# Performance work log

Measured on AMD Instinct MI355X. Metric: run time of the kernel, lower is better.

Reference implementation:

```python
import jax, jax.numpy as jnp
import numpy as np

T, N, HIDDEN = 2048, 4, 512
N_HEAD = 8
D_HEAD = HIDDEN // N_HEAD
# Faithful to torch buffer: 1.0 / hidden_size ** d_head -> underflows to 0.0
SCALE = np.float32(1.0 / (HIDDEN ** D_HEAD))
LN_EPS = 1e-5


def _layernorm(x, g, b):
    m = jnp.mean(x, axis=-1, keepdims=True)
    v = jnp.mean(jnp.square(x - m), axis=-1, keepdims=True)
    return (x - m) * jax.lax.rsqrt(v + LN_EPS) * g + b


def setup_inputs() -> dict:
    key = jax.random.key(0)
    ks = jax.random.split(key, 6)
    s = 0.02
    return {
        "x": jax.random.normal(ks[0], (T, N, HIDDEN), jnp.float32),
        "qkv_w": jax.random.normal(ks[1], (HIDDEN, 3 * HIDDEN), jnp.float32) * s,
        "qkv_b": jnp.zeros((3 * HIDDEN,), jnp.float32),
        "out_w": jax.random.normal(ks[2], (HIDDEN, HIDDEN), jnp.float32) * s,
        "out_b": jnp.zeros((HIDDEN,), jnp.float32),
        "ln1_g": jnp.ones((HIDDEN,), jnp.float32),
        "ln1_b": jnp.zeros((HIDDEN,), jnp.float32),
        "ff1_w": jax.random.normal(ks[3], (HIDDEN, 2 * HIDDEN), jnp.float32) * s,
        "ff1_b": jnp.zeros((2 * HIDDEN,), jnp.float32),
        "ff2_w": jax.random.normal(ks[4], (2 * HIDDEN, HIDDEN), jnp.float32) * s,
        "ff2_b": jnp.zeros((HIDDEN,), jnp.float32),
        "ln2_g": jnp.ones((HIDDEN,), jnp.float32),
        "ln2_b": jnp.zeros((HIDDEN,), jnp.float32),
    }


def reference(x, qkv_w, qkv_b, out_w, out_b, ln1_g, ln1_b,
              ff1_w, ff1_b, ff2_w, ff2_b, ln2_g, ln2_b):
    t, n, _ = x.shape
    # prenorm=True path, dropout_p=0 (identity)
    residual = x
    h = _layernorm(x, ln1_g, ln1_b)
    qkv = h @ qkv_w + qkv_b  # [t, n, 3*hidden]
    q, k, v = jnp.split(qkv, 3, axis=2)
    q = q.reshape(t, n, N_HEAD, D_HEAD)
    k = k.reshape(t, n, N_HEAD, D_HEAD)
    v = v.reshape(t, n, N_HEAD, D_HEAD)
    logits = jnp.einsum('ibhd,jbhd->ijbh', q, k)
    probs = jax.nn.softmax(logits * SCALE, axis=1)
    attn_out = jnp.einsum('ijbh,jbhd->ibhd', probs, v).reshape(t, n, HIDDEN)
    x = residual + (attn_out @ out_w + out_b)
    residual = x
    h = _layernorm(x, ln2_g, ln2_b)
    ff = jnp.maximum(h @ ff1_w + ff1_b, 0.0) @ ff2_w + ff2_b
    return residual + ff
```

## Files before the change

### kernel.cpp

```cpp
#include <hip/hip_runtime.h>
#include <math.h>


#define DEVI __device__ __forceinline__

typedef unsigned short u16;
typedef unsigned int   u32;
using short8 = __attribute__((ext_vector_type(8))) short;
using f32x4  = __attribute__((ext_vector_type(4))) float;

constexpr int T_ = 2048;
constexpr int NB = 4;
constexpr int H  = 512;
constexpr int M  = T_ * NB;
constexpr int FF = 2 * H;
constexpr float LN_EPS = 1e-5f;
constexpr int NCHUNK = 256;

DEVI u16 f2bf(float f) {
    union { float f; u32 u; } v; v.f = f;
    u32 r = v.u + 0x7FFFu + ((v.u >> 16) & 1u);
    return (u16)(r >> 16);
}
DEVI float bf2f(u16 h) {
    union { u32 u; float f; } v; v.u = ((u32)h) << 16; return v.f;
}

DEVI void gload16(const u16* src, u16* lds) {
    __builtin_amdgcn_global_load_lds(
        (const __attribute__((address_space(1))) u32*)src,
        (__attribute__((address_space(3))) u32*)lds, 16, 0, 0);
}

DEVI float hsum8(const float4& a, const float4& b) {
    return a.x + a.y + a.z + a.w + b.x + b.y + b.z + b.w;
}
DEVI float hsq8(const float4& a, const float4& b) {
    return a.x*a.x + a.y*a.y + a.z*a.z + a.w*a.w +
           b.x*b.x + b.y*b.y + b.z*b.z + b.w*b.w;
}
DEVI float4 ln_apply(const float4& v, float mean, float rs,
                     const float4& g, const float4& b) {
    float4 r;
    r.x = (v.x - mean) * rs * g.x + b.x;
    r.y = (v.y - mean) * rs * g.y + b.y;
    r.z = (v.z - mean) * rs * g.z + b.z;
    r.w = (v.w - mean) * rs * g.w + b.w;
    return r;
}
DEVI void add4(float4& a, const float4& b) {
    a.x += b.x; a.y += b.y; a.z += b.z; a.w += b.w;
}
DEVI void wave_reduce2(float& s, float& q) {
    #pragma unroll
    for (int m = 1; m < 64; m <<= 1) {
        s += __shfl_xor(s, m, 64);
        q += __shfl_xor(q, m, 64);
    }
}

__global__ __launch_bounds__(256) void k_ln1_partial(
    const float* __restrict__ x, const float* __restrict__ g,
    const float* __restrict__ be, float* __restrict__ partials)
{
    const int lane = threadIdx.x & 63;
    const int w    = threadIdx.x >> 6;
    const int t0   = blockIdx.x * 8;

    const float4* G4 = (const float4*)g;
    const float4* B4 = (const float4*)be;
    const float4 g0 = G4[lane], g1 = G4[64 + lane];
    const float4 b0 = B4[lane], b1 = B4[64 + lane];

    float4 acc0 = {0, 0, 0, 0}, acc1 = {0, 0, 0, 0};
    for (int i = 0; i < 8; ++i) {
        const int r = (t0 + i) * NB + w;
        const float4* X4 = (const float4*)(x + (size_t)r * H);
        float4 v0 = X4[lane], v1 = X4[64 + lane];
        float s = hsum8(v0, v1);
        float q = hsq8(v0, v1);
        wave_reduce2(s, q);
        const float mean = s * (1.0f / H);
        const float var  = q * (1.0f / H) - mean * mean;
        const float rs   = 1.0f / sqrtf(var + LN_EPS);
        add4(acc0, ln_apply(v0, mean, rs, g0, b0));
        add4(acc1, ln_apply(v1, mean, rs, g1, b1));
    }
    float4* P4 = (float4*)(partials + ((size_t)w * NCHUNK + blockIdx.x) * H);
    P4[lane]      = acc0;
    P4[64 + lane] = acc1;
}

__global__ void k_reduce_mean(const float* __restrict__ partials,
                              float* __restrict__ mean_h1)
{
    const int tid = blockIdx.x * blockDim.x + threadIdx.x;
    const int b = tid >> 9;
    const int e = tid & 511;
    float s = 0.f;
    for (int c = 0; c < NCHUNK; ++c)
        s += partials[((size_t)b * NCHUNK + c) * H + e];
    mean_h1[tid] = s * (1.0f / T_);
}

__global__ __launch_bounds__(256) void k_gemv_wave(
    const float* __restrict__ vec, const float* __restrict__ W,
    const float* __restrict__ bias, float* __restrict__ outv,
    const int Kd, const int rowstride, const int colofs)
{
    const int wid  = blockIdx.x * 4 + (threadIdx.x >> 6);
    const int lane = threadIdx.x & 63;
    const int b = wid >> 9;
    const int j = wid & 511;
    const float* v  = vec + (size_t)b * Kd;
    const float* wc = W + colofs + j;
    float s = 0.f;
    for (int i = 0; i < Kd / 64; ++i) {
        const int k = i * 64 + lane;
        s = fmaf(v[k], wc[(size_t)k * rowstride], s);
    }
    #pragma unroll
    for (int m = 1; m < 64; m <<= 1) s += __shfl_xor(s, m, 64);
    if (lane == 0) outv[wid] = s + bias[j];
}

__global__ __launch_bounds__(256) void k_ln2(
    const float* __restrict__ x, const float* __restrict__ cvec,
    const float* __restrict__ g, const float* __restrict__ be,
    u16* __restrict__ h2bf)
{
    const int lane = threadIdx.x & 63;
    const int w    = threadIdx.x >> 6;
    const int r    = blockIdx.x * 4 + w;
    const int b    = r & 3;

    const float4* X4 = (const float4*)(x + (size_t)r * H);
    const float4* C4 = (const float4*)(cvec + (size_t)b * H);
    float4 v0 = X4[lane], v1 = X4[64 + lane];
    add4(v0, C4[lane]);
    add4(v1, C4[64 + lane]);

    float s = hsum8(v0, v1);
    float q = hsq8(v0, v1);
    wave_reduce2(s, q);
    const float mean = s * (1.0f / H);
    const float var  = q * (1.0f / H) - mean * mean;
    const float rs   = 1.0f / sqrtf(var + LN_EPS);

    const float4* G4 = (const float4*)g;
    const float4* B4 = (const float4*)be;
    float4 h0 = ln_apply(v0, mean, rs, G4[lane],      B4[lane]);
    float4 h1 = ln_apply(v1, mean, rs, G4[64 + lane], B4[64 + lane]);

    u16* row = h2bf + (size_t)r * H;
    *(ushort4*)&row[lane * 4]       = make_ushort4(f2bf(h0.x), f2bf(h0.y), f2bf(h0.z), f2bf(h0.w));
    *(ushort4*)&row[256 + lane * 4] = make_ushort4(f2bf(h1.x), f2bf(h1.y), f2bf(h1.z), f2bf(h1.w));
}

__global__ __launch_bounds__(256) void k_wsplit(
    const float* __restrict__ W, u16* __restrict__ Whi, u16* __restrict__ Wlo,
    const int K, const int N)
{
    __shared__ float tile[32][33];
    const int kt = blockIdx.x * 32, nt = blockIdx.y * 32;
    const int t = threadIdx.x;
    #pragma unroll
    for (int i = 0; i < 4; ++i) {
        const int idx = t + i * 256;
        const int r = idx >> 5, c = idx & 31;
        tile[r][c] = W[(size_t)(kt + r) * N + nt + c];
    }
    __syncthreads();
    #pragma unroll
    for (int i = 0; i < 4; ++i) {
        const int idx = t + i * 256;
        const int r = idx >> 5, c = idx & 31;
        const float v = tile[c][r];
        const u16 hi = f2bf(v);
        const u16 lo = f2bf(v - bf2f(hi));
        const size_t o = (size_t)(nt + r) * K + kt + c;
        Whi[o] = hi;
        Wlo[o] = lo;
    }
}

template<int BM, int BN, int MODE>
__global__ __launch_bounds__(256) void gemm_bf16(
    const u16* __restrict__ Abf, const u16* __restrict__ Bhi,
    const u16* __restrict__ Blo, const float* __restrict__ bias,
    const float* __restrict__ resid_x, const float* __restrict__ resid_c,
    float* __restrict__ outf, u16* __restrict__ outbf,
    const int K, const int N)
{
    constexpr int BK = 32;
    constexpr int WM = BM / 2, WN = BN / 2;
    constexpr int FM = WM / 16, FN = WN / 16;
    __shared__ alignas(16) u16 As[BM * BK];
    __shared__ alignas(16) u16 Bh[BN * BK];
    __shared__ alignas(16) u16 Bl[BN * BK];

    const int t    = threadIdx.x;
    const int lane = t & 63, w = t >> 6;
    const int wr = w >> 1, wc = w & 1;
    const int lr = lane & 15, lk = lane >> 4;
    const int bm0 = blockIdx.x * BM, bn0 = blockIdx.y * BN;

    f32x4 acc[FM][FN];
    #pragma unroll
    for (int i = 0; i < FM; ++i)
        #pragma unroll
        for (int j = 0; j < FN; ++j)
            acc[i][j] = (f32x4){0.f, 0.f, 0.f, 0.f};

    for (int k0 = 0; k0 < K; k0 += BK) {
        __syncthreads();
        #pragma unroll
        for (int c = 0; c < BM / 64; ++c) {
            const int flat = c * 256 + t;
            const int row = flat >> 2, kb = (flat & 3) * 8;
            gload16(Abf + (size_t)(bm0 + row) * K + k0 + kb, &As[flat * 8]);
        }
        #pragma unroll
        for (int c = 0; c < BN / 64; ++c) {
            const int flat = c * 256 + t;
            const int row = flat >> 2, kb = (flat & 3) * 8;
            gload16(Bhi + (size_t)(bn0 + row) * K + k0 + kb, &Bh[flat * 8]);
            gload16(Blo + (size_t)(bn0 + row) * K + k0 + kb, &Bl[flat * 8]);
        }
        __syncthreads();

        short8 af[FM], bh[FN], bl[FN];
        #pragma unroll
        for (int i = 0; i < FM; ++i)
            af[i] = *(const short8*)&As[(wr * WM + i * 16 + lr) * BK + lk * 8];
        #pragma unroll
        for (int j = 0; j < FN; ++j) {
            bh[j] = *(const short8*)&Bh[(wc * WN + j * 16 + lr) * BK + lk * 8];
            bl[j] = *(const short8*)&Bl[(wc * WN + j * 16 + lr) * BK + lk * 8];
        }
        #pragma unroll
        for (int i = 0; i < FM; ++i)
            #pragma unroll
            for (int j = 0; j < FN; ++j)
                acc[i][j] = __builtin_amdgcn_mfma_f32_16x16x32_bf16(
                    af[i], bh[j], acc[i][j], 0, 0, 0);
        #pragma unroll
        for (int i = 0; i < FM; ++i)
            #pragma unroll
            for (int j = 0; j < FN; ++j)
                acc[i][j] = __builtin_amdgcn_mfma_f32_16x16x32_bf16(
                    af[i], bl[j], acc[i][j], 0, 0, 0);
    }

    #pragma unroll
    for (int i = 0; i < FM; ++i) {
        const int row0 = bm0 + wr * WM + i * 16 + lk * 4;
        #pragma unroll
        for (int j = 0; j < FN; ++j) {
            const int col = bn0 + wc * WN + j * 16 + lr;
            #pragma unroll
            for (int r = 0; r < 4; ++r) {
                const int row = row0 + r;
                float v = acc[i][j][r] + bias[col];
                if (MODE == 0) {
                    v = fmaxf(v, 0.f);
                    outbf[(size_t)row * N + col] = f2bf(v);
                } else {
                    v += resid_x[(size_t)row * N + col]
                       + resid_c[(row & 3) * N + col];
                    outf[(size_t)row * N + col] = v;
                }
            }
        }
    }
}

extern "C" void kernel_launch(void* const* d_in, const int* in_sizes, int n_in,
                              void* d_out, int out_size, void* d_ws, size_t ws_size,
                              hipStream_t stream)
{
    const float* x     = (const float*)d_in[0];
    const float* qkv_w = (const float*)d_in[1];
    const float* qkv_b = (const float*)d_in[2];
    const float* out_w = (const float*)d_in[3];
    const float* out_b = (const float*)d_in[4];
    const float* ln1_g = (const float*)d_in[5];
    const float* ln1_b = (const float*)d_in[6];
    const float* ff1_w = (const float*)d_in[7];
    const float* ff1_b = (const float*)d_in[8];
    const float* ff2_w = (const float*)d_in[9];
    const float* ff2_b = (const float*)d_in[10];
    const float* ln2_g = (const float*)d_in[11];
    const float* ln2_b = (const float*)d_in[12];

    float* out = (float*)d_out;

    float* fws      = (float*)d_ws;
    float* partials = fws;
    float* mh       = fws + (size_t)4 * NCHUNK * H;
    float* vmean    = mh + NB * H;
    float* cvec     = vmean + NB * H;
    u16*   h2bf     = (u16*)(cvec + NB * H);
    u16*   f1bf     = h2bf + (size_t)M * H;
    u16*   w1hi     = f1bf + (size_t)M * FF;
    u16*   w1lo     = w1hi + (size_t)H * FF;
    u16*   w2hi     = w1lo + (size_t)H * FF;
    u16*   w2lo     = w2hi + (size_t)FF * H;

    k_wsplit<<<dim3(H / 32, FF / 32), 256, 0, stream>>>(ff1_w, w1hi, w1lo, H, FF);
    k_wsplit<<<dim3(FF / 32, H / 32), 256, 0, stream>>>(ff2_w, w2hi, w2lo, FF, H);

    k_ln1_partial<<<NCHUNK, 256, 0, stream>>>(x, ln1_g, ln1_b, partials);
    k_reduce_mean<<<8, 256, 0, stream>>>(partials, mh);
    k_gemv_wave<<<512, 256, 0, stream>>>(mh, qkv_w, qkv_b + 2 * H, vmean,
                                         H, 3 * H, 2 * H);
    k_gemv_wave<<<512, 256, 0, stream>>>(vmean, out_w, out_b, cvec,
                                         H, H, 0);

    k_ln2<<<M / 4, 256, 0, stream>>>(x, cvec, ln2_g, ln2_b, h2bf);

    gemm_bf16<128, 128, 0><<<dim3(M / 128, FF / 128), 256, 0, stream>>>(
        h2bf, w1hi, w1lo, ff1_b, nullptr, nullptr, nullptr, f1bf, H, FF);

    gemm_bf16<64, 128, 1><<<dim3(M / 64, H / 128), 256, 0, stream>>>(
        f1bf, w2hi, w2lo, ff2_b, x, cvec, out, nullptr, FF, H);
}
```

Measured before the change: 179.5 us.

## Use MFMA fragment-major layouts, drop bf16 lo weight split, retune GEMV/reduce

Activations and weights are now written in a pre-swizzled 16x32 MFMA fragment-major layout, so GEMM tiles load contiguous fragments and LDS reads are one short8 per lane. The bf16 hi/lo weight split is removed, which halves both the B-operand traffic and the MFMA count. The GEMM moves to 128x128 tiles with BK=64 for both stages. The mean reduction and GEMV kernels are restructured: the reduction is split across 8 lanes with shuffles, and the GEMV uses one thread per output with the vector in LDS. Dropping the lo term lowers weight precision to plain bf16, and the GEMV now runs on only 8 blocks, which may underutilize the GPU.

```diff
diff --git a/kernel.cpp b/kernel.cpp
--- a/kernel.cpp
+++ b/kernel.cpp
@@ -21,9 +21,6 @@
     union { float f; u32 u; } v; v.f = f;
     u32 r = v.u + 0x7FFFu + ((v.u >> 16) & 1u);
     return (u16)(r >> 16);
-}
-DEVI float bf2f(u16 h) {
-    union { u32 u; float f; } v; v.u = ((u32)h) << 16; return v.f;
 }
 
 DEVI void gload16(const u16* src, u16* lds) {
@@ -91,43 +88,49 @@
     P4[64 + lane] = acc1;
 }
 
-__global__ void k_reduce_mean(const float* __restrict__ partials,
-                              float* __restrict__ mean_h1)
-{
-    const int tid = blockIdx.x * blockDim.x + threadIdx.x;
-    const int b = tid >> 9;
-    const int e = tid & 511;
+__global__ __launch_bounds__(256) void k_reduce_mean(
+    const float* __restrict__ partials, float* __restrict__ mean_h1)
+{
+    const int tid = blockIdx.x * 256 + threadIdx.x;
+    const int out = tid >> 3;
+    const int sub = tid & 7;
+    const int b = out >> 9;
+    const int e = out & 511;
     float s = 0.f;
-    for (int c = 0; c < NCHUNK; ++c)
+    #pragma unroll 8
+    for (int i = 0; i < 32; ++i) {
+        const int c = sub * 32 + i;
         s += partials[((size_t)b * NCHUNK + c) * H + e];
-    mean_h1[tid] = s * (1.0f / T_);
-}
-
-__global__ __launch_bounds__(256) void k_gemv_wave(
+    }
+    s += __shfl_xor(s, 1, 64);
+    s += __shfl_xor(s, 2, 64);
+    s += __shfl_xor(s, 4, 64);
+    if (sub == 0) mean_h1[out] = s * (1.0f / T_);
+}
+
+__global__ __launch_bounds__(256) void k_gemv_tpo(
     const float* __restrict__ vec, const float* __restrict__ W,
     const float* __restrict__ bias, float* __restrict__ outv,
     const int Kd, const int rowstride, const int colofs)
 {
-    const int wid  = blockIdx.x * 4 + (threadIdx.x >> 6);
-    const int lane = threadIdx.x & 63;
-    const int b = wid >> 9;
-    const int j = wid & 511;
-    const float* v  = vec + (size_t)b * Kd;
-    const float* wc = W + colofs + j;
-    float s = 0.f;
-    for (int i = 0; i < Kd / 64; ++i) {
-        const int k = i * 64 + lane;
-        s = fmaf(v[k], wc[(size_t)k * rowstride], s);
-    }
-    #pragma unroll
-    for (int m = 1; m < 64; m <<= 1) s += __shfl_xor(s, m, 64);
-    if (lane == 0) outv[wid] = s + bias[j];
+    __shared__ float v[512];
+    const int t = threadIdx.x;
+    const int b = blockIdx.x >> 1;
+    const int j = (blockIdx.x & 1) * 256 + t;
+    for (int i = t; i < Kd; i += 256) v[i] = vec[(size_t)b * Kd + i];
+    __syncthreads();
+    float acc = bias[j];
+    const float* wp = W + colofs + j;
+    #pragma unroll 8
+    for (int k = 0; k < Kd; ++k)
+        acc = fmaf(v[k], wp[(size_t)k * rowstride], acc);
+    outv[(size_t)b * 512 + j] = acc;
 }
 
 __global__ __launch_bounds__(256) void k_ln2(
     const float* __restrict__ x, const float* __restrict__ cvec,
     const float* __restrict__ g, const float* __restrict__ be,
-    u16* __restrict__ h2bf)
+    u16* __restrict__ h2f)
 {
     const int lane = threadIdx.x & 63;
     const int w    = threadIdx.x >> 6;
@@ -136,9 +139,9 @@
 
     const float4* X4 = (const float4*)(x + (size_t)r * H);
     const float4* C4 = (const float4*)(cvec + (size_t)b * H);
-    float4 v0 = X4[lane], v1 = X4[64 + lane];
-    add4(v0, C4[lane]);
-    add4(v1, C4[64 + lane]);
+    float4 v0 = X4[lane * 2],     v1 = X4[lane * 2 + 1];
+    add4(v0, C4[lane * 2]);
+    add4(v1, C4[lane * 2 + 1]);
 
     float s = hsum8(v0, v1);
     float q = hsq8(v0, v1);
@@ -149,122 +152,129 @@
 
     const float4* G4 = (const float4*)g;
     const float4* B4 = (const float4*)be;
-    float4 h0 = ln_apply(v0, mean, rs, G4[lane],      B4[lane]);
-    float4 h1 = ln_apply(v1, mean, rs, G4[64 + lane], B4[64 + lane]);
-
-    u16* row = h2bf + (size_t)r * H;
-    *(ushort4*)&row[lane * 4]       = make_ushort4(f2bf(h0.x), f2bf(h0.y), f2bf(h0.z), f2bf(h0.w));
-    *(ushort4*)&row[256 + lane * 4] = make_ushort4(f2bf(h1.x), f2bf(h1.y), f2bf(h1.z), f2bf(h1.w));
+    float4 h0 = ln_apply(v0, mean, rs, G4[lane * 2],     B4[lane * 2]);
+    float4 h1 = ln_apply(v1, mean, rs, G4[lane * 2 + 1], B4[lane * 2 + 1]);
+
+    short8 o;
+    o[0] = f2bf(h0.x); o[1] = f2bf(h0.y); o[2] = f2bf(h0.z); o[3] = f2bf(h0.w);
+    o[4] = f2bf(h1.x); o[5] = f2bf(h1.y); o[6] = f2bf(h1.z); o[7] = f2bf(h1.w);
+
+    const size_t idx = (((size_t)(r >> 4) * 16 + (lane >> 2)) << 9)
+                     + ((lane & 3) * 16 + (r & 15)) * 8;
+    *(short8*)&h2f[idx] = o;
 }
 
 __global__ __launch_bounds__(256) void k_wsplit(
-    const float* __restrict__ W, u16* __restrict__ Whi, u16* __restrict__ Wlo,
+    const float* __restrict__ W, u16* __restrict__ Wf,
     const int K, const int N)
 {
     __shared__ float tile[32][33];
-    const int kt = blockIdx.x * 32, nt = blockIdx.y * 32;
+    const int k0 = blockIdx.x * 32, n0 = blockIdx.y * 32;
     const int t = threadIdx.x;
+    const int KT = K >> 5;
     #pragma unroll
     for (int i = 0; i < 4; ++i) {
         const int idx = t + i * 256;
         const int r = idx >> 5, c = idx & 31;
-        tile[r][c] = W[(size_t)(kt + r) * N + nt + c];
+        tile[r][c] = W[(size_t)(k0 + r) * N + n0 + c];
     }
     __syncthreads();
-    #pragma unroll
-    for (int i = 0; i < 4; ++i) {
-        const int idx = t + i * 256;
-        const int r = idx >> 5, c = idx & 31;
-        const float v = tile[c][r];
-        const u16 hi = f2bf(v);
-        const u16 lo = f2bf(v - bf2f(hi));
-        const size_t o = (size_t)(nt + r) * K + kt + c;
-        Whi[o] = hi;
-        Wlo[o] = lo;
-    }
-}
-
-template<int BM, int BN, int MODE>
+    if (t < 128) {
+        const int tt = t >> 6;
+        const int c  = t & 63;
+        short8 o;
+        #pragma unroll
+        for (int kin = 0; kin < 8; ++kin)
+            o[kin] = f2bf(tile[(c >> 4) * 8 + kin][tt * 16 + (c & 15)]);
+        const size_t idx = (((size_t)(n0 / 16 + tt) * KT + (k0 >> 5)) << 9)
+                         + c * 8;
+        *(short8*)&Wf[idx] = o;
+    }
+}
+
+template<int MODE>
 __global__ __launch_bounds__(256) void gemm_bf16(
-    const u16* __restrict__ Abf, const u16* __restrict__ Bhi,
-    const u16* __restrict__ Blo, const float* __restrict__ bias,
+    const u16* __restrict__ Af, const u16* __restrict__ Bf,
+    const float* __restrict__ bias,
     const float* __restrict__ resid_x, const float* __restrict__ resid_c,
-    float* __restrict__ outf, u16* __restrict__ outbf,
+    float* __restrict__ outf, u16* __restrict__ outfrag,
     const int K, const int N)
 {
-    constexpr int BK = 32;
-    constexpr int WM = BM / 2, WN = BN / 2;
-    constexpr int FM = WM / 16, FN = WN / 16;
+    constexpr int BM = 128, BN = 128, BK = 64;
+    const int KT = K >> 5;
     __shared__ alignas(16) u16 As[BM * BK];
-    __shared__ alignas(16) u16 Bh[BN * BK];
-    __shared__ alignas(16) u16 Bl[BN * BK];
+    __shared__ alignas(16) u16 Bs[BN * BK];
 
     const int t    = threadIdx.x;
     const int lane = t & 63, w = t >> 6;
     const int wr = w >> 1, wc = w & 1;
     const int lr = lane & 15, lk = lane >> 4;
-    const int bm0 = blockIdx.x * BM, bn0 = blockIdx.y * BN;
-
-    f32x4 acc[FM][FN];
+    const int bmt = blockIdx.x * 8;
+    const int bnt = blockIdx.y * 8;
+
+    f32x4 acc[4][4];
     #pragma unroll
-    for (int i = 0; i < FM; ++i)
-        #pragma unroll
-        for (int j = 0; j < FN; ++j)
+    for (int i = 0; i < 4; ++i)
+        #pragma unroll
+        for (int j = 0; j < 4; ++j)
             acc[i][j] = (f32x4){0.f, 0.f, 0.f, 0.f};
 
-    for (int k0 = 0; k0 < K; k0 += BK) {
+    for (int kt0 = 0; kt0 < KT; kt0 += 2) {
         __syncthreads();
         #pragma unroll
-        for (int c = 0; c < BM / 64; ++c) {
-            const int flat = c * 256 + t;
-            const int row = flat >> 2, kb = (flat & 3) * 8;
-            gload16(Abf + (size_t)(bm0 + row) * K + k0 + kb, &As[flat * 8]);
+        for (int ft = 0; ft < 4; ++ft) {
+            const int f = ft * 256 + t;
+            const int mt = f >> 7, ktl = (f >> 6) & 1, c = f & 63;
+            gload16(Af + (((size_t)(bmt + mt) * KT + kt0 + ktl) << 9) + c * 8,
+                    &As[f * 8]);
         }
         #pragma unroll
-        for (int c = 0; c < BN / 64; ++c) {
-            const int flat = c * 256 + t;
-            const int row = flat >> 2, kb = (flat & 3) * 8;
-            gload16(Bhi + (size_t)(bn0 + row) * K + k0 + kb, &Bh[flat * 8]);
-            gload16(Blo + (size_t)(bn0 + row) * K + k0 + kb, &Bl[flat * 8]);
+        for (int ft = 0; ft < 4; ++ft) {
+            const int f = ft * 256 + t;
+            const int nt = f >> 7, ktl = (f >> 6) & 1, c = f & 63;
+            gload16(Bf + (((size_t)(bnt + nt) * KT + kt0 + ktl) << 9) + c * 8,
+                    &Bs[f * 8]);
         }
         __syncthreads();
 
-        short8 af[FM], bh[FN], bl[FN];
-        #pragma unroll
-        for (int i = 0; i < FM; ++i)
-            af[i] = *(const short8*)&As[(wr * WM + i * 16 + lr) * BK + lk * 8];
-        #pragma unroll
-        for (int j = 0; j < FN; ++j) {
-            bh[j] = *(const short8*)&Bh[(wc * WN + j * 16 + lr) * BK + lk * 8];
-            bl[j] = *(const short8*)&Bl[(wc * WN + j * 16 + lr) * BK + lk * 8];
+        #pragma unroll
+        for (int ktl = 0; ktl < 2; ++ktl) {
+            short8 a[4], b[4];
+            #pragma unroll
+            for (int i = 0; i < 4; ++i)
+                a[i] = *(const short8*)&As[(((wr * 4 + i) * 2 + ktl) << 9) + lane * 8];
+            #pragma unroll
+            for (int j = 0; j < 4; ++j)
+                b[j] = *(const short8*)&Bs[(((wc * 4 + j) * 2 + ktl) << 9) + lane * 8];
+            #pragma unroll
+            for (int i = 0; i < 4; ++i)
+                #pragma unroll
+                for (int j = 0; j < 4; ++j)
+                    acc[i][j] = __builtin_amdgcn_mfma_f32_16x16x32_bf16(
+                        a[i], b[j], acc[i][j], 0, 0, 0);
         }
-        #pragma unroll
-        for (int i = 0; i < FM; ++i)
-            #pragma unroll
-            for (int j = 0; j < FN; ++j)
-                acc[i][j] = __builtin_amdgcn_mfma_f32_16x16x32_bf16(
-                    af[i], bh[j], acc[i][j], 0, 0, 0);
-        #pragma unroll
-        for (int i = 0; i < FM; ++i)
-            #pragma unroll
-            for (int j = 0; j < FN; ++j)
-                acc[i][j] = __builtin_amdgcn_mfma_f32_16x16x32_bf16(
-                    af[i], bl[j], acc[i][j], 0, 0, 0);
-    }
-
+    }
+
+    const int K2T = N >> 5;
     #pragma unroll
-    for (int i = 0; i < FM; ++i) {
-        const int row0 = bm0 + wr * WM + i * 16 + lk * 4;
-        #pragma unroll
-        for (int j = 0; j < FN; ++j) {
-            const int col = bn0 + wc * WN + j * 16 + lr;
+    for (int i = 0; i < 4; ++i) {
+        const int rt   = bmt + wr * 4 + i;
+        const int row0 = rt * 16 + lk * 4;
+        #pragma unroll
+        for (int j = 0; j < 4; ++j) {
+            const int col = (bnt + wc * 4 + j) * 16 + lr;
+            const float bv = bias[col];
             #pragma unroll
             for (int r = 0; r < 4; ++r) {
                 const int row = row0 + r;
-                float v = acc[i][j][r] + bias[col];
+                float v = acc[i][j][r] + bv;
                 if (MODE == 0) {
                     v = fmaxf(v, 0.f);
-                    outbf[(size_t)row * N + col] = f2bf(v);
+                    const size_t idx =
+                        (((size_t)rt * K2T + (col >> 5)) << 9)
+                        + (((col >> 3) & 3) * 16 + (lk * 4 + r)) * 8
+                        + (col & 7);
+                    outfrag[idx] = f2bf(v);
                 } else {
                     v += resid_x[(size_t)row * N + col]
                        + resid_c[(row & 3) * N + col];
@@ -300,28 +310,26 @@
     float* mh       = fws + (size_t)4 * NCHUNK * H;
     float* vmean    = mh + NB * H;
     float* cvec     = vmean + NB * H;
-    u16*   h2bf     = (u16*)(cvec + NB * H);
-    u16*   f1bf     = h2bf + (size_t)M * H;
-    u16*   w1hi     = f1bf + (size_t)M * FF;
-    u16*   w1lo     = w1hi + (size_t)H * FF;
-    u16*   w2hi     = w1lo + (size_t)H * FF;
-    u16*   w2lo     = w2hi + (size_t)FF * H;
-
-    k_wsplit<<<dim3(H / 32, FF / 32), 256, 0, stream>>>(ff1_w, w1hi, w1lo, H, FF);
-    k_wsplit<<<dim3(FF / 32, H / 32), 256, 0, stream>>>(ff2_w, w2hi, w2lo, FF, H);
+    u16*   h2f      = (u16*)(cvec + NB * H);
+    u16*   f1f      = h2f + (size_t)M * H;
+    u16*   w1f      = f1f + (size_t)M * FF;
+    u16*   w2f      = w1f + (size_t)H * FF;
+
+    k_wsplit<<<dim3(H / 32, FF / 32), 256, 0, stream>>>(ff1_w, w1f, H, FF);
+    k_wsplit<<<dim3(FF / 32, H / 32), 256, 0, stream>>>(ff2_w, w2f, FF, H);
 
     k_ln1_partial<<<NCHUNK, 256, 0, stream>>>(x, ln1_g, ln1_b, partials);
-    k_reduce_mean<<<8, 256, 0, stream>>>(partials, mh);
-    k_gemv_wave<<<512, 256, 0, stream>>>(mh, qkv_w, qkv_b + 2 * H, vmean,
-                                         H, 3 * H, 2 * H);
-    k_gemv_wave<<<512, 256, 0, stream>>>(vmean, out_w, out_b, cvec,
-                                         H, H, 0);
-
-    k_ln2<<<M / 4, 256, 0, stream>>>(x, cvec, ln2_g, ln2_b, h2bf);
-
-    gemm_bf16<128, 128, 0><<<dim3(M / 128, FF / 128), 256, 0, stream>>>(
-        h2bf, w1hi, w1lo, ff1_b, nullptr, nullptr, nullptr, f1bf, H, FF);
-
-    gemm_bf16<64, 128, 1><<<dim3(M / 64, H / 128), 256, 0, stream>>>(
-        f1bf, w2hi, w2lo, ff2_b, x, cvec, out, nullptr, FF, H);
-}
+    k_reduce_mean<<<64, 256, 0, stream>>>(partials, mh);
+    k_gemv_tpo<<<8, 256, 0, stream>>>(mh, qkv_w, qkv_b + 2 * H, vmean,
+                                      H, 3 * H, 2 * H);
+    k_gemv_tpo<<<8, 256, 0, stream>>>(vmean, out_w, out_b, cvec,
+                                      H, H, 0);
+
+    k_ln2<<<M / 4, 256, 0, stream>>>(x, cvec, ln2_g, ln2_b, h2f);
+
+    gemm_bf16<0><<<dim3(M / 128, FF / 128), 256, 0, stream>>>(
+        h2f, w1f, ff1_b, nullptr, nullptr, nullptr, f1f, H, FF);
+
+    gemm_bf16<1><<<dim3(M / 128, H / 128), 256, 0, stream>>>(
+        f1f, w2f, ff2_b, x, cvec, out, nullptr, FF, H);
+}
```

New measurement: 199.0 us. 1.11x slower.
